# Optimization experiments

Measured on AMD Instinct MI355X. Metric: run time of the kernel, lower is better.

Reference implementation:

```python
import jax, jax.numpy as jnp
import numpy as np

D_HIST = 64
LO, HI = -3.0, 3.0
FALL_OFF = 0.02
EPS = 1e-6


def setup_inputs() -> dict:
    key = jax.random.key(0)
    k1, k2 = jax.random.split(key)
    x = jax.random.uniform(k1, (8, 3, 256, 256), dtype=jnp.float32)
    y = jax.random.uniform(k2, (8, 3, 256, 256), dtype=jnp.float32)
    return {"x": x, "y": y}


def _hist_feature(img):
    # img: (B, 3, H, W)
    B = img.shape[0]
    flat = (img + EPS).reshape(B, 3, -1)            # (B, 3, N)
    i_y = jnp.sqrt(jnp.sum(jnp.square(flat), axis=1))  # (B, N) pixel intensity
    lr, lg, lb = jnp.log(flat[:, 0]), jnp.log(flat[:, 1]), jnp.log(flat[:, 2])
    ur = lr - lg
    vr = lr - lb
    ug, vg = -ur, -ur + vr
    ub, vb = -vr, -vr + ur
    centers = jnp.linspace(LO, HI, D_HIST, dtype=img.dtype)  # (D,)

    def rbf(d):
        # inverse-quadratic kernel vs bin centers -> (B, N, D)
        return 1.0 / (1.0 + jnp.square(jnp.abs(d[..., None] - centers) / FALL_OFF))

    def hist_c(uc, vc):
        # weighted outer-product reduction over pixels (the bmm): (B, D, D)
        return jnp.einsum('bn,bnu,bnv->buv', i_y, rbf(uc), rbf(vc))

    hist = jnp.stack([hist_c(ur, vr), hist_c(ug, vg), hist_c(ub, vb)], axis=1)  # (B,3,D,D)
    total = jnp.sum(hist, axis=(1, 2, 3), keepdims=True)
    return hist / total


def reference(x, y):
    x_hist = _hist_feature(x)
    y_hist = _hist_feature(y)
    diff = jnp.sqrt(y_hist) - jnp.sqrt(x_hist)
    h = jnp.sum(jnp.square(diff), axis=(1, 2, 3))  # (B,)
    h_norm = jnp.sqrt(h) * jnp.sqrt(jnp.asarray(0.5, dtype=h.dtype))
    return jnp.mean(h_norm)
```

## Files before the change

kernel.cpp:

```cpp
#include <hip/hip_runtime.h>
#include <math.h>

#define N_PIX 65536
#define EPSF 1e-6f
#define CHUNKS 32
#define PX_PER_CHUNK 2048
#define PX_PER_WAVE 512
#define N_TILES (PX_PER_WAVE / 64)
#define N_JOBS 48
#define N_BLOCKS (N_JOBS * CHUNKS)
#define N_RBLOCKS (24 * 4)
#define LN2_50 34.65735903f

typedef __attribute__((ext_vector_type(2))) float f2;
using short8 = __attribute__((ext_vector_type(8))) short;
using f32x4  = __attribute__((ext_vector_type(4))) float;

__device__ __forceinline__ float rcp_fast(float x) { return __builtin_amdgcn_rcpf(x); }

#if __has_builtin(__builtin_amdgcn_cvt_pk_bf16_f32)
typedef __attribute__((ext_vector_type(2))) __bf16 bf16x2_t;
__device__ __forceinline__ uint32_t pk_bf16(float a, float b) {
    return __builtin_bit_cast(uint32_t, __builtin_amdgcn_cvt_pk_bf16_f32(a, b));
}
#else
__device__ __forceinline__ uint32_t pk_bf16(float a, float b) {
    const uint32_t ua = __builtin_bit_cast(uint32_t, a) + 0x8000u;
    const uint32_t ub = __builtin_bit_cast(uint32_t, b) + 0x8000u;
    return __builtin_amdgcn_perm(ub, ua, 0x07060302u);
}
#endif

__device__ __forceinline__ float4 phaseA(float pr, float pg, float pb, int c) {
    const float r  = pr + EPSF;
    const float g  = pg + EPSF;
    const float bl = pb + EPSF;
    const float wgt = sqrtf(fmaf(r, r, fmaf(g, g, bl * bl)));
    const float lr = __log2f(r), lg = __log2f(g), lb2 = __log2f(bl);
    const float l0 = (c == 0) ? lr : ((c == 1) ? lg : lb2);
    const float lu = (c == 0) ? lg : lr;
    const float lv = (c == 2) ? lg : lb2;
    return make_float4((l0 - lu) * LN2_50, (l0 - lv) * LN2_50, wgt, 0.0f);
}

__global__ __launch_bounds__(256, 4) void hist_kernel(
    const float* __restrict__ x, const float* __restrict__ y,
    float* __restrict__ partial, float* __restrict__ accum)
{
    const int blk = blockIdx.x;
    const int chunk = blk & (CHUNKS - 1);
    const int job = blk / CHUNKS;
    const int c = job % 3;
    const int ib = job / 3;
    const int img = ib >> 3;
    const int b = ib & 7;
    const float* __restrict__ src = (img == 0 ? x : y) + (size_t)b * 3 * N_PIX;

    const int tid = threadIdx.x;
    if (blk == 0 && tid < 25) ((unsigned*)accum)[tid] = 0u;

    __shared__ __align__(16) float lds[4096];
    const int lane = tid & 63;
    const int wv = tid >> 6;
    float* __restrict__ wbuf = lds + wv * 288;

    const int quad = lane >> 4;
    const int l15 = lane & 15;
    f2 ncb01, ncb23;
    {
        const float c0 = (-3.0f + (float)(l15)      * (6.0f / 63.0f)) * 50.0f;
        const float c1 = (-3.0f + (float)(16 + l15) * (6.0f / 63.0f)) * 50.0f;
        const float c2 = (-3.0f + (float)(32 + l15) * (6.0f / 63.0f)) * 50.0f;
        const float c3 = (-3.0f + (float)(48 + l15) * (6.0f / 63.0f)) * 50.0f;
        ncb01 = (f2){-c0, -c1};
        ncb23 = (f2){-c2, -c3};
    }
    const f2 one2 = {1.0f, 1.0f};

    f32x4 acc[16];
#pragma unroll
    for (int i = 0; i < 16; ++i) acc[i] = (f32x4){0.f, 0.f, 0.f, 0.f};

    const int px0 = chunk * PX_PER_CHUNK + wv * PX_PER_WAVE;

    float pr, pg, pb;
    {
        const int n = px0 + lane;
        pr = src[n]; pg = src[N_PIX + n]; pb = src[2 * N_PIX + n];
    }

#pragma unroll 1
    for (int st = 0; st < N_TILES; ++st) {
        const float4 uvw = phaseA(pr, pg, pb, c);
        *(float4*)(wbuf + lane * 4 + (lane >> 3) * 4) = uvw;

        if (st + 1 < N_TILES) {
            const int n2 = px0 + (st + 1) * 64 + lane;
            pr = src[n2]; pg = src[N_PIX + n2]; pb = src[2 * N_PIX + n2];
        }

#pragma unroll
        for (int h = 0; h < 2; ++h) {
            const int base = h * 32 + quad * 8;
            const float4* __restrict__ pbase =
                (const float4*)(wbuf + base * 4 + (base >> 3) * 4);
            int aU[4][4], aV[4][4];

#pragma unroll
            for (int jp = 0; jp < 4; ++jp) {
                const float4 pe = pbase[2 * jp];
                const float4 po = pbase[2 * jp + 1];

                f2 aue01, aue23, auo01, auo23;
                f2 bve01, bve23, bvo01, bvo23;
#pragma unroll
                for (int eo = 0; eo < 2; ++eo) {
                    const float ru = eo ? po.x : pe.x;
                    const float rv = eo ? po.y : pe.y;
                    const float rw = eo ? po.z : pe.z;
                    const f2 ru2 = {ru, ru}, rv2 = {rv, rv}, rw2 = {rw, rw};
                    const f2 tu01 = ru2 + ncb01, tu23 = ru2 + ncb23;
                    const f2 tv01 = rv2 + ncb01, tv23 = rv2 + ncb23;
                    const f2 qu01 = __builtin_elementwise_fma(tu01, tu01, one2);
                    const f2 qu23 = __builtin_elementwise_fma(tu23, tu23, one2);
                    const f2 qv01 = __builtin_elementwise_fma(tv01, tv01, one2);
                    const f2 qv23 = __builtin_elementwise_fma(tv23, tv23, one2);
                    const f2 au01 = (f2){rcp_fast(qu01.x), rcp_fast(qu01.y)} * rw2;
                    const f2 au23 = (f2){rcp_fast(qu23.x), rcp_fast(qu23.y)} * rw2;
                    const f2 bv01 = {rcp_fast(qv01.x), rcp_fast(qv01.y)};
                    const f2 bv23 = {rcp_fast(qv23.x), rcp_fast(qv23.y)};
                    if (eo) { auo01 = au01; auo23 = au23; bvo01 = bv01; bvo23 = bv23; }
                    else    { aue01 = au01; aue23 = au23; bve01 = bv01; bve23 = bv23; }
                }
                aU[0][jp] = pk_bf16(aue01.x, auo01.x);
                aU[1][jp] = pk_bf16(aue01.y, auo01.y);
                aU[2][jp] = pk_bf16(aue23.x, auo23.x);
                aU[3][jp] = pk_bf16(aue23.y, auo23.y);
                aV[0][jp] = pk_bf16(bve01.x, bvo01.x);
                aV[1][jp] = pk_bf16(bve01.y, bvo01.y);
                aV[2][jp] = pk_bf16(bve23.x, bvo23.x);
                aV[3][jp] = pk_bf16(bve23.y, bvo23.y);
            }

            short8 af[4], bf[4];
#pragma unroll
            for (int mt = 0; mt < 4; ++mt) {
                af[mt] = __builtin_bit_cast(short8,
                    make_int4(aU[mt][0], aU[mt][1], aU[mt][2], aU[mt][3]));
                bf[mt] = __builtin_bit_cast(short8,
                    make_int4(aV[mt][0], aV[mt][1], aV[mt][2], aV[mt][3]));
            }
#pragma unroll
            for (int mt = 0; mt < 4; ++mt)
#pragma unroll
                for (int nt = 0; nt < 4; ++nt)
                    acc[mt * 4 + nt] = __builtin_amdgcn_mfma_f32_16x16x32_bf16(
                        af[mt], bf[nt], acc[mt * 4 + nt], 0, 0, 0);
        }
    }

    float* __restrict__ outp = partial + (size_t)blk * 4096;
#pragma unroll 1
    for (int ch = 0; ch < 4; ++ch) {
        __syncthreads();
#pragma unroll
        for (int nt = 0; nt < 4; ++nt)
            *(f32x4*)(lds + wv * 1024 + nt * 256 + lane * 4) = acc[ch * 4 + nt];
        __syncthreads();
        const int e4 = tid * 4;
        const f32x4 s0 = *(const f32x4*)(lds +        e4);
        const f32x4 s1 = *(const f32x4*)(lds + 1024 + e4);
        const f32x4 s2 = *(const f32x4*)(lds + 2048 + e4);
        const f32x4 s3 = *(const f32x4*)(lds + 3072 + e4);
        const f32x4 s = (s0 + s1) + (s2 + s3);
        *(f32x4*)(outp + ch * 1024 + e4) = s;
    }
}

__global__ __launch_bounds__(256) void reduce_cross_kernel(
    const float* __restrict__ partial, float* __restrict__ accum,
    float* __restrict__ out)
{
    unsigned* __restrict__ ticket = (unsigned*)(accum + 24);
    const int jx = blockIdx.x >> 2;
    const int bb = jx / 3;
    const int e4 = (((blockIdx.x & 3) << 8) | threadIdx.x) * 4;
    const float* px = partial + (size_t)jx * CHUNKS * 4096 + e4;
    const float* py = partial + (size_t)(24 + jx) * CHUNKS * 4096 + e4;

    f32x4 qx = {0.f, 0.f, 0.f, 0.f}, qy = {0.f, 0.f, 0.f, 0.f};
#pragma unroll 8
    for (int k = 0; k < CHUNKS; ++k) {
        qx += *(const f32x4*)(px + (size_t)k * 4096);
        qy += *(const f32x4*)(py + (size_t)k * 4096);
    }
    float sx = (qx.x + qx.y) + (qx.z + qx.w);
    float sy = (qy.x + qy.y) + (qy.z + qy.w);
    float cr = (sqrtf(qx.x * qy.x) + sqrtf(qx.y * qy.y)) +
               (sqrtf(qx.z * qy.z) + sqrtf(qx.w * qy.w));

#pragma unroll
    for (int o = 32; o > 0; o >>= 1) {
        sx += __shfl_down(sx, o, 64);
        sy += __shfl_down(sy, o, 64);
        cr += __shfl_down(cr, o, 64);
    }
    __shared__ float red[12];
    const int wv = threadIdx.x >> 6;
    if ((threadIdx.x & 63) == 0) {
        red[wv] = sx; red[4 + wv] = sy; red[8 + wv] = cr;
    }
    __syncthreads();
    if (threadIdx.x == 0) {
        atomicAdd(&accum[bb],      red[0] + red[1] + red[2] + red[3]);
        atomicAdd(&accum[8 + bb],  red[4] + red[5] + red[6] + red[7]);
        atomicAdd(&accum[16 + bb], red[8] + red[9] + red[10] + red[11]);
        const unsigned old = __hip_atomic_fetch_add(ticket, 1u,
                                 __ATOMIC_ACQ_REL, __HIP_MEMORY_SCOPE_AGENT);
        if (old == N_RBLOCKS - 1) {
            float s = 0.0f;
#pragma unroll
            for (int b = 0; b < 8; ++b) {
                const float tx = __hip_atomic_load(&accum[b],      __ATOMIC_ACQUIRE, __HIP_MEMORY_SCOPE_AGENT);
                const float ty = __hip_atomic_load(&accum[8 + b],  __ATOMIC_ACQUIRE, __HIP_MEMORY_SCOPE_AGENT);
                const float cc = __hip_atomic_load(&accum[16 + b], __ATOMIC_ACQUIRE, __HIP_MEMORY_SCOPE_AGENT);
                const float rho = cc * __builtin_amdgcn_rsqf(tx * ty);
                s += sqrtf(fmaxf(1.0f - rho, 0.0f));
            }
            out[0] = s * 0.125f;
        }
    }
}

extern "C" void kernel_launch(void* const* d_in, const int* in_sizes, int n_in,
                              void* d_out, int out_size, void* d_ws, size_t ws_size,
                              hipStream_t stream)
{
    const float* x = (const float*)d_in[0];
    const float* y = (const float*)d_in[1];
    float* ws = (float*)d_ws;
    float* partial = ws;
    float* accum = ws + (size_t)N_BLOCKS * 4096;
    float* outf = (float*)d_out;

    hipLaunchKernelGGL(hist_kernel, dim3(N_BLOCKS), dim3(256), 0, stream,
                       x, y, partial, accum);
    hipLaunchKernelGGL(reduce_cross_kernel, dim3(N_RBLOCKS), dim3(256), 0, stream,
                       partial, accum, outf);
}
```

Measured before the change: 149.2 us.

## Split histogram output columns across waves and share U-side RBF tiles via LDS

Each wave now owns a 16-column slice of the 64x64 histogram, so it computes only one bin center's RBF values per pixel instead of four. The weighted U-side fragments are exchanged through double-buffered LDS across the four waves with block-level barriers. This removes the redundant 4x RBF/reciprocal work per wave, the cross-wave LDS reduction at the end, and most of the accumulator registers, which allows a higher occupancy target. In exchange it adds many __syncthreads and LDS traffic per macro-tile of 256 pixels.

```diff
diff --git a/kernel.cpp b/kernel.cpp
--- a/kernel.cpp
+++ b/kernel.cpp
@@ -5,8 +5,8 @@
 #define EPSF 1e-6f
 #define CHUNKS 32
 #define PX_PER_CHUNK 2048
-#define PX_PER_WAVE 512
-#define N_TILES (PX_PER_WAVE / 64)
+#define MACRO_PX 256
+#define N_MACROS 8
 #define N_JOBS 48
 #define N_BLOCKS (N_JOBS * CHUNKS)
 #define N_RBLOCKS (24 * 4)
@@ -43,7 +43,7 @@
     return make_float4((l0 - lu) * LN2_50, (l0 - lv) * LN2_50, wgt, 0.0f);
 }
 
-__global__ __launch_bounds__(256, 4) void hist_kernel(
+__global__ __launch_bounds__(256, 6) void hist_kernel(
     const float* __restrict__ x, const float* __restrict__ y,
     float* __restrict__ partial, float* __restrict__ accum)
 {
@@ -59,122 +59,112 @@
     const int tid = threadIdx.x;
     if (blk == 0 && tid < 25) ((unsigned*)accum)[tid] = 0u;
 
-    __shared__ __align__(16) float lds[4096];
+    __shared__ __align__(16) float uvw_lds[2][1152];
+    __shared__ __align__(16) int   af_lds[2][2048];
+
     const int lane = tid & 63;
     const int wv = tid >> 6;
-    float* __restrict__ wbuf = lds + wv * 288;
-
     const int quad = lane >> 4;
     const int l15 = lane & 15;
-    f2 ncb01, ncb23;
-    {
-        const float c0 = (-3.0f + (float)(l15)      * (6.0f / 63.0f)) * 50.0f;
-        const float c1 = (-3.0f + (float)(16 + l15) * (6.0f / 63.0f)) * 50.0f;
-        const float c2 = (-3.0f + (float)(32 + l15) * (6.0f / 63.0f)) * 50.0f;
-        const float c3 = (-3.0f + (float)(48 + l15) * (6.0f / 63.0f)) * 50.0f;
-        ncb01 = (f2){-c0, -c1};
-        ncb23 = (f2){-c2, -c3};
-    }
+
+    const float cc = (-3.0f + (float)(wv * 16 + l15) * (6.0f / 63.0f)) * 50.0f;
+    const f2 nc2 = {-cc, -cc};
     const f2 one2 = {1.0f, 1.0f};
 
-    f32x4 acc[16];
-#pragma unroll
-    for (int i = 0; i < 16; ++i) acc[i] = (f32x4){0.f, 0.f, 0.f, 0.f};
-
-    const int px0 = chunk * PX_PER_CHUNK + wv * PX_PER_WAVE;
+    f32x4 acc[4];
+#pragma unroll
+    for (int i = 0; i < 4; ++i) acc[i] = (f32x4){0.f, 0.f, 0.f, 0.f};
+
+    const int px0 = chunk * PX_PER_CHUNK;
 
     float pr, pg, pb;
     {
-        const int n = px0 + lane;
+        const int n = px0 + wv * 64 + lane;
         pr = src[n]; pg = src[N_PIX + n]; pb = src[2 * N_PIX + n];
     }
 
-#pragma unroll 1
-    for (int st = 0; st < N_TILES; ++st) {
-        const float4 uvw = phaseA(pr, pg, pb, c);
-        *(float4*)(wbuf + lane * 4 + (lane >> 3) * 4) = uvw;
-
-        if (st + 1 < N_TILES) {
-            const int n2 = px0 + (st + 1) * 64 + lane;
-            pr = src[n2]; pg = src[N_PIX + n2]; pb = src[2 * N_PIX + n2];
-        }
-
+    short8 bfh0, bfh1;
+
+    auto produce = [&](const float* __restrict__ ub, int s) {
+        const int bufsel = s & 1;
 #pragma unroll
         for (int h = 0; h < 2; ++h) {
-            const int base = h * 32 + quad * 8;
+            const int pxb = s * 64 + h * 32 + quad * 8;
             const float4* __restrict__ pbase =
-                (const float4*)(wbuf + base * 4 + (base >> 3) * 4);
-            int aU[4][4], aV[4][4];
-
+                (const float4*)(ub + pxb * 4 + (pxb >> 3) * 4);
+            int aw[4], bw[4];
 #pragma unroll
             for (int jp = 0; jp < 4; ++jp) {
                 const float4 pe = pbase[2 * jp];
                 const float4 po = pbase[2 * jp + 1];
-
-                f2 aue01, aue23, auo01, auo23;
-                f2 bve01, bve23, bvo01, bvo23;
-#pragma unroll
-                for (int eo = 0; eo < 2; ++eo) {
-                    const float ru = eo ? po.x : pe.x;
-                    const float rv = eo ? po.y : pe.y;
-                    const float rw = eo ? po.z : pe.z;
-                    const f2 ru2 = {ru, ru}, rv2 = {rv, rv}, rw2 = {rw, rw};
-                    const f2 tu01 = ru2 + ncb01, tu23 = ru2 + ncb23;
-                    const f2 tv01 = rv2 + ncb01, tv23 = rv2 + ncb23;
-                    const f2 qu01 = __builtin_elementwise_fma(tu01, tu01, one2);
-                    const f2 qu23 = __builtin_elementwise_fma(tu23, tu23, one2);
-                    const f2 qv01 = __builtin_elementwise_fma(tv01, tv01, one2);
-                    const f2 qv23 = __builtin_elementwise_fma(tv23, tv23, one2);
-                    const f2 au01 = (f2){rcp_fast(qu01.x), rcp_fast(qu01.y)} * rw2;
-                    const f2 au23 = (f2){rcp_fast(qu23.x), rcp_fast(qu23.y)} * rw2;
-                    const f2 bv01 = {rcp_fast(qv01.x), rcp_fast(qv01.y)};
-                    const f2 bv23 = {rcp_fast(qv23.x), rcp_fast(qv23.y)};
-                    if (eo) { auo01 = au01; auo23 = au23; bvo01 = bv01; bvo23 = bv23; }
-                    else    { aue01 = au01; aue23 = au23; bve01 = bv01; bve23 = bv23; }
-                }
-                aU[0][jp] = pk_bf16(aue01.x, auo01.x);
-                aU[1][jp] = pk_bf16(aue01.y, auo01.y);
-                aU[2][jp] = pk_bf16(aue23.x, auo23.x);
-                aU[3][jp] = pk_bf16(aue23.y, auo23.y);
-                aV[0][jp] = pk_bf16(bve01.x, bvo01.x);
-                aV[1][jp] = pk_bf16(bve01.y, bvo01.y);
-                aV[2][jp] = pk_bf16(bve23.x, bvo23.x);
-                aV[3][jp] = pk_bf16(bve23.y, bvo23.y);
+                const f2 ru2 = {pe.x, po.x};
+                const f2 rv2 = {pe.y, po.y};
+                const f2 rw2 = {pe.z, po.z};
+                const f2 tu = ru2 + nc2;
+                const f2 tv = rv2 + nc2;
+                const f2 qu = __builtin_elementwise_fma(tu, tu, one2);
+                const f2 qv = __builtin_elementwise_fma(tv, tv, one2);
+                const f2 au = (f2){rcp_fast(qu.x), rcp_fast(qu.y)} * rw2;
+                aw[jp] = (int)pk_bf16(au.x, au.y);
+                bw[jp] = (int)pk_bf16(rcp_fast(qv.x), rcp_fast(qv.y));
             }
-
-            short8 af[4], bf[4];
-#pragma unroll
-            for (int mt = 0; mt < 4; ++mt) {
+            *(int4*)(&af_lds[bufsel][h * 1024 + wv * 256 + lane * 4]) =
+                make_int4(aw[0], aw[1], aw[2], aw[3]);
+            const short8 bwv =
+                __builtin_bit_cast(short8, make_int4(bw[0], bw[1], bw[2], bw[3]));
+            if (h == 0) bfh0 = bwv; else bfh1 = bwv;
+        }
+    };
+    auto consume = [&](int s) {
+        const int bufsel = s & 1;
+#pragma unroll
+        for (int h = 0; h < 2; ++h) {
+            short8 af[4];
+#pragma unroll
+            for (int mt = 0; mt < 4; ++mt)
                 af[mt] = __builtin_bit_cast(short8,
-                    make_int4(aU[mt][0], aU[mt][1], aU[mt][2], aU[mt][3]));
-                bf[mt] = __builtin_bit_cast(short8,
-                    make_int4(aV[mt][0], aV[mt][1], aV[mt][2], aV[mt][3]));
-            }
+                    *(const int4*)(&af_lds[bufsel][h * 1024 + mt * 256 + lane * 4]));
+            const short8 bh = (h == 0) ? bfh0 : bfh1;
 #pragma unroll
             for (int mt = 0; mt < 4; ++mt)
-#pragma unroll
-                for (int nt = 0; nt < 4; ++nt)
-                    acc[mt * 4 + nt] = __builtin_amdgcn_mfma_f32_16x16x32_bf16(
-                        af[mt], bf[nt], acc[mt * 4 + nt], 0, 0, 0);
-        }
-    }
-
-    float* __restrict__ outp = partial + (size_t)blk * 4096;
+                acc[mt] = __builtin_amdgcn_mfma_f32_16x16x32_bf16(
+                    af[mt], bh, acc[mt], 0, 0, 0);
+        }
+    };
+
 #pragma unroll 1
-    for (int ch = 0; ch < 4; ++ch) {
-        __syncthreads();
-#pragma unroll
-        for (int nt = 0; nt < 4; ++nt)
-            *(f32x4*)(lds + wv * 1024 + nt * 256 + lane * 4) = acc[ch * 4 + nt];
-        __syncthreads();
-        const int e4 = tid * 4;
-        const f32x4 s0 = *(const f32x4*)(lds +        e4);
-        const f32x4 s1 = *(const f32x4*)(lds + 1024 + e4);
-        const f32x4 s2 = *(const f32x4*)(lds + 2048 + e4);
-        const f32x4 s3 = *(const f32x4*)(lds + 3072 + e4);
-        const f32x4 s = (s0 + s1) + (s2 + s3);
-        *(f32x4*)(outp + ch * 1024 + e4) = s;
-    }
+    for (int m = 0; m < N_MACROS; ++m) {
+        {
+            const float4 uvw = phaseA(pr, pg, pb, c);
+            const int pxw = wv * 64 + lane;
+            *(float4*)(&uvw_lds[m & 1][pxw * 4 + (pxw >> 3) * 4]) = uvw;
+        }
+        __syncthreads();
+
+        float nr = 0.f, ng = 0.f, nb = 0.f;
+        if (m + 1 < N_MACROS) {
+            const int n2 = px0 + (m + 1) * 256 + wv * 64 + lane;
+            nr = src[n2]; ng = src[N_PIX + n2]; nb = src[2 * N_PIX + n2];
+        }
+
+        const float* __restrict__ ub = &uvw_lds[m & 1][0];
+        produce(ub, 0);
+        __syncthreads();
+        consume(0); produce(ub, 1);
+        __syncthreads();
+        consume(1); produce(ub, 2);
+        __syncthreads();
+        consume(2); produce(ub, 3);
+        __syncthreads();
+        consume(3);
+
+        pr = nr; pg = ng; pb = nb;
+    }
+
+    float* __restrict__ outp = partial + (size_t)blk * 4096 + wv * 1024;
+#pragma unroll
+    for (int mt = 0; mt < 4; ++mt)
+        *(f32x4*)(outp + mt * 256 + lane * 4) = acc[mt];
 }
 
 __global__ __launch_bounds__(256) void reduce_cross_kernel(
```

New measurement: 154.7 us. 3.7% more time.

## Fuse cross-chunk reduction into histogram kernel via per-job last-block tickets

Applied to the files above, without the earlier changes.

Drops the separate reduction kernel. Each x/y job pair now gets a ticket counter, and the last of its 64 chunk blocks sums the partials and adds the Bhattacridge-style cross terms to the per-batch accumulators. A final ticket computes the output. The job index is remapped so x and y jobs for the same batch and channel sit next to each other. Accumulators are now zeroed with a memset before launch. This removes one kernel launch and its tail, but the reduction for each pair runs serially in a single block and adds a memset.

```diff
diff --git a/kernel.cpp b/kernel.cpp
--- a/kernel.cpp
+++ b/kernel.cpp
@@ -9,7 +9,6 @@
 #define N_TILES (PX_PER_WAVE / 64)
 #define N_JOBS 48
 #define N_BLOCKS (N_JOBS * CHUNKS)
-#define N_RBLOCKS (24 * 4)
 #define LN2_50 34.65735903f
 
 typedef __attribute__((ext_vector_type(2))) float f2;
@@ -45,21 +44,23 @@
 
 __global__ __launch_bounds__(256, 4) void hist_kernel(
     const float* __restrict__ x, const float* __restrict__ y,
-    float* __restrict__ partial, float* __restrict__ accum)
+    float* __restrict__ partial, float* __restrict__ accum,
+    float* __restrict__ out)
 {
     const int blk = blockIdx.x;
     const int chunk = blk & (CHUNKS - 1);
     const int job = blk / CHUNKS;
-    const int c = job % 3;
-    const int ib = job / 3;
-    const int img = ib >> 3;
-    const int b = ib & 7;
+    const int img = job & 1;
+    const int jp  = job >> 1;
+    const int c = jp % 3;
+    const int b = jp / 3;
     const float* __restrict__ src = (img == 0 ? x : y) + (size_t)b * 3 * N_PIX;
 
     const int tid = threadIdx.x;
-    if (blk == 0 && tid < 25) ((unsigned*)accum)[tid] = 0u;
 
     __shared__ __align__(16) float lds[4096];
+    __shared__ float red[12];
+    __shared__ unsigned last_flag;
     const int lane = tid & 63;
     const int wv = tid >> 6;
     float* __restrict__ wbuf = lds + wv * 288;
@@ -107,9 +108,9 @@
             int aU[4][4], aV[4][4];
 
 #pragma unroll
-            for (int jp = 0; jp < 4; ++jp) {
-                const float4 pe = pbase[2 * jp];
-                const float4 po = pbase[2 * jp + 1];
+            for (int jj = 0; jj < 4; ++jj) {
+                const float4 pe = pbase[2 * jj];
+                const float4 po = pbase[2 * jj + 1];
 
                 f2 aue01, aue23, auo01, auo23;
                 f2 bve01, bve23, bvo01, bvo23;
@@ -132,14 +133,14 @@
                     if (eo) { auo01 = au01; auo23 = au23; bvo01 = bv01; bvo23 = bv23; }
                     else    { aue01 = au01; aue23 = au23; bve01 = bv01; bve23 = bv23; }
                 }
-                aU[0][jp] = pk_bf16(aue01.x, auo01.x);
-                aU[1][jp] = pk_bf16(aue01.y, auo01.y);
-                aU[2][jp] = pk_bf16(aue23.x, auo23.x);
-                aU[3][jp] = pk_bf16(aue23.y, auo23.y);
-                aV[0][jp] = pk_bf16(bve01.x, bvo01.x);
-                aV[1][jp] = pk_bf16(bve01.y, bvo01.y);
-                aV[2][jp] = pk_bf16(bve23.x, bvo23.x);
-                aV[3][jp] = pk_bf16(bve23.y, bvo23.y);
+                aU[0][jj] = pk_bf16(aue01.x, auo01.x);
+                aU[1][jj] = pk_bf16(aue01.y, auo01.y);
+                aU[2][jj] = pk_bf16(aue23.x, auo23.x);
+                aU[3][jj] = pk_bf16(aue23.y, auo23.y);
+                aV[0][jj] = pk_bf16(bve01.x, bvo01.x);
+                aV[1][jj] = pk_bf16(bve01.y, bvo01.y);
+                aV[2][jj] = pk_bf16(bve23.x, bvo23.x);
+                aV[3][jj] = pk_bf16(bve23.y, bvo23.y);
             }
 
             short8 af[4], bf[4];
@@ -175,59 +176,64 @@
         const f32x4 s = (s0 + s1) + (s2 + s3);
         *(f32x4*)(outp + ch * 1024 + e4) = s;
     }
-}
-
-__global__ __launch_bounds__(256) void reduce_cross_kernel(
-    const float* __restrict__ partial, float* __restrict__ accum,
-    float* __restrict__ out)
-{
-    unsigned* __restrict__ ticket = (unsigned*)(accum + 24);
-    const int jx = blockIdx.x >> 2;
-    const int bb = jx / 3;
-    const int e4 = (((blockIdx.x & 3) << 8) | threadIdx.x) * 4;
-    const float* px = partial + (size_t)jx * CHUNKS * 4096 + e4;
-    const float* py = partial + (size_t)(24 + jx) * CHUNKS * 4096 + e4;
-
-    f32x4 qx = {0.f, 0.f, 0.f, 0.f}, qy = {0.f, 0.f, 0.f, 0.f};
-#pragma unroll 8
-    for (int k = 0; k < CHUNKS; ++k) {
-        qx += *(const f32x4*)(px + (size_t)k * 4096);
-        qy += *(const f32x4*)(py + (size_t)k * 4096);
-    }
-    float sx = (qx.x + qx.y) + (qx.z + qx.w);
-    float sy = (qy.x + qy.y) + (qy.z + qy.w);
-    float cr = (sqrtf(qx.x * qy.x) + sqrtf(qx.y * qy.y)) +
-               (sqrtf(qx.z * qy.z) + sqrtf(qx.w * qy.w));
-
-#pragma unroll
-    for (int o = 32; o > 0; o >>= 1) {
-        sx += __shfl_down(sx, o, 64);
-        sy += __shfl_down(sy, o, 64);
-        cr += __shfl_down(cr, o, 64);
-    }
-    __shared__ float red[12];
-    const int wv = threadIdx.x >> 6;
-    if ((threadIdx.x & 63) == 0) {
-        red[wv] = sx; red[4 + wv] = sy; red[8 + wv] = cr;
-    }
+
     __syncthreads();
-    if (threadIdx.x == 0) {
-        atomicAdd(&accum[bb],      red[0] + red[1] + red[2] + red[3]);
-        atomicAdd(&accum[8 + bb],  red[4] + red[5] + red[6] + red[7]);
-        atomicAdd(&accum[16 + bb], red[8] + red[9] + red[10] + red[11]);
-        const unsigned old = __hip_atomic_fetch_add(ticket, 1u,
+    unsigned* __restrict__ pticket = (unsigned*)(accum + 24);
+    if (tid == 0) {
+        const unsigned old = __hip_atomic_fetch_add(&pticket[jp], 1u,
                                  __ATOMIC_ACQ_REL, __HIP_MEMORY_SCOPE_AGENT);
-        if (old == N_RBLOCKS - 1) {
-            float s = 0.0f;
-#pragma unroll
-            for (int b = 0; b < 8; ++b) {
-                const float tx = __hip_atomic_load(&accum[b],      __ATOMIC_ACQUIRE, __HIP_MEMORY_SCOPE_AGENT);
-                const float ty = __hip_atomic_load(&accum[8 + b],  __ATOMIC_ACQUIRE, __HIP_MEMORY_SCOPE_AGENT);
-                const float cc = __hip_atomic_load(&accum[16 + b], __ATOMIC_ACQUIRE, __HIP_MEMORY_SCOPE_AGENT);
-                const float rho = cc * __builtin_amdgcn_rsqf(tx * ty);
-                s += sqrtf(fmaxf(1.0f - rho, 0.0f));
-            }
-            out[0] = s * 0.125f;
+        last_flag = (old == 63u) ? 1u : 0u;
+    }
+    __syncthreads();
+    if (last_flag) {
+        const float* __restrict__ px = partial + (size_t)(2 * jp) * CHUNKS * 4096;
+        const float* __restrict__ py = px + (size_t)CHUNKS * 4096;
+        float sx = 0.f, sy = 0.f, cr = 0.f;
+#pragma unroll 1
+        for (int s = 0; s < 4; ++s) {
+            const int e4 = tid * 4 + s * 1024;
+            const float* __restrict__ pxe = px + e4;
+            const float* __restrict__ pye = py + e4;
+            f32x4 qx = {0.f, 0.f, 0.f, 0.f}, qy = {0.f, 0.f, 0.f, 0.f};
+#pragma unroll 4
+            for (int k = 0; k < CHUNKS; ++k) {
+                qx += *(const f32x4*)(pxe + (size_t)k * 4096);
+                qy += *(const f32x4*)(pye + (size_t)k * 4096);
+            }
+            sx += (qx.x + qx.y) + (qx.z + qx.w);
+            sy += (qy.x + qy.y) + (qy.z + qy.w);
+            cr += (sqrtf(qx.x * qy.x) + sqrtf(qx.y * qy.y)) +
+                  (sqrtf(qx.z * qy.z) + sqrtf(qx.w * qy.w));
+        }
+#pragma unroll
+        for (int o = 32; o > 0; o >>= 1) {
+            sx += __shfl_down(sx, o, 64);
+            sy += __shfl_down(sy, o, 64);
+            cr += __shfl_down(cr, o, 64);
+        }
+        if ((tid & 63) == 0) {
+            red[wv] = sx; red[4 + wv] = sy; red[8 + wv] = cr;
+        }
+        __syncthreads();
+        if (tid == 0) {
+            atomicAdd(&accum[b],      red[0] + red[1] + red[2] + red[3]);
+            atomicAdd(&accum[8 + b],  red[4] + red[5] + red[6] + red[7]);
+            atomicAdd(&accum[16 + b], red[8] + red[9] + red[10] + red[11]);
+            unsigned* __restrict__ fin = (unsigned*)(accum + 48);
+            const unsigned old = __hip_atomic_fetch_add(fin, 1u,
+                                     __ATOMIC_ACQ_REL, __HIP_MEMORY_SCOPE_AGENT);
+            if (old == 23u) {
+                float sum = 0.0f;
+#pragma unroll
+                for (int bb = 0; bb < 8; ++bb) {
+                    const float tx = __hip_atomic_load(&accum[bb],      __ATOMIC_ACQUIRE, __HIP_MEMORY_SCOPE_AGENT);
+                    const float ty = __hip_atomic_load(&accum[8 + bb],  __ATOMIC_ACQUIRE, __HIP_MEMORY_SCOPE_AGENT);
+                    const float cc = __hip_atomic_load(&accum[16 + bb], __ATOMIC_ACQUIRE, __HIP_MEMORY_SCOPE_AGENT);
+                    const float rho = cc * __builtin_amdgcn_rsqf(tx * ty);
+                    sum += sqrtf(fmaxf(1.0f - rho, 0.0f));
+                }
+                out[0] = sum * 0.125f;
+            }
         }
     }
 }
@@ -243,8 +249,7 @@
     float* accum = ws + (size_t)N_BLOCKS * 4096;
     float* outf = (float*)d_out;
 
+    hipMemsetAsync(accum, 0, 49 * sizeof(float), stream);
     hipLaunchKernelGGL(hist_kernel, dim3(N_BLOCKS), dim3(256), 0, stream,
-                       x, y, partial, accum);
-    hipLaunchKernelGGL(reduce_cross_kernel, dim3(N_RBLOCKS), dim3(256), 0, stream,
-                       partial, accum, outf);
-}
+                       x, y, partial, accum, outf);
+}
```

Result: slower. 219.0 us (+46.8%).

## Accumulate per-chunk histograms atomically into a few slots per job

Applied to the files above, without the earlier changes.

Each hist block now atomically adds its 4096-bin partial histogram into one of 4 slots per job, where it used to write its own private partial buffer. The reduce kernel then reads only 4 slots per job instead of 32 chunks, which shrinks partial-buffer memory traffic. The cost is a memset of the slot buffer before the histogram kernel, plus global float atomics with contention from 8 blocks per slot. Float atomics also make the summation order nondeterministic.

```diff
diff --git a/kernel.cpp b/kernel.cpp
--- a/kernel.cpp
+++ b/kernel.cpp
@@ -9,6 +9,7 @@
 #define N_TILES (PX_PER_WAVE / 64)
 #define N_JOBS 48
 #define N_BLOCKS (N_JOBS * CHUNKS)
+#define SLOTS 4
 #define N_RBLOCKS (24 * 4)
 #define LN2_50 34.65735903f
 
@@ -45,7 +46,7 @@
 
 __global__ __launch_bounds__(256, 4) void hist_kernel(
     const float* __restrict__ x, const float* __restrict__ y,
-    float* __restrict__ partial, float* __restrict__ accum)
+    float* __restrict__ jobacc, float* __restrict__ accum)
 {
     const int blk = blockIdx.x;
     const int chunk = blk & (CHUNKS - 1);
@@ -57,7 +58,6 @@
     const float* __restrict__ src = (img == 0 ? x : y) + (size_t)b * 3 * N_PIX;
 
     const int tid = threadIdx.x;
-    if (blk == 0 && tid < 25) ((unsigned*)accum)[tid] = 0u;
 
     __shared__ __align__(16) float lds[4096];
     const int lane = tid & 63;
@@ -159,7 +159,8 @@
         }
     }
 
-    float* __restrict__ outp = partial + (size_t)blk * 4096;
+    float* __restrict__ outp =
+        jobacc + ((size_t)job * SLOTS + (chunk & (SLOTS - 1))) * 4096;
 #pragma unroll 1
     for (int ch = 0; ch < 4; ++ch) {
         __syncthreads();
@@ -173,26 +174,30 @@
         const f32x4 s2 = *(const f32x4*)(lds + 2048 + e4);
         const f32x4 s3 = *(const f32x4*)(lds + 3072 + e4);
         const f32x4 s = (s0 + s1) + (s2 + s3);
-        *(f32x4*)(outp + ch * 1024 + e4) = s;
+        float* __restrict__ dst = outp + ch * 1024 + e4;
+        atomicAdd(dst + 0, s.x);
+        atomicAdd(dst + 1, s.y);
+        atomicAdd(dst + 2, s.z);
+        atomicAdd(dst + 3, s.w);
     }
 }
 
 __global__ __launch_bounds__(256) void reduce_cross_kernel(
-    const float* __restrict__ partial, float* __restrict__ accum,
+    const float* __restrict__ jobacc, float* __restrict__ accum,
     float* __restrict__ out)
 {
     unsigned* __restrict__ ticket = (unsigned*)(accum + 24);
     const int jx = blockIdx.x >> 2;
     const int bb = jx / 3;
     const int e4 = (((blockIdx.x & 3) << 8) | threadIdx.x) * 4;
-    const float* px = partial + (size_t)jx * CHUNKS * 4096 + e4;
-    const float* py = partial + (size_t)(24 + jx) * CHUNKS * 4096 + e4;
+    const float* px = jobacc + (size_t)jx * SLOTS * 4096 + e4;
+    const float* py = jobacc + (size_t)(24 + jx) * SLOTS * 4096 + e4;
 
     f32x4 qx = {0.f, 0.f, 0.f, 0.f}, qy = {0.f, 0.f, 0.f, 0.f};
-#pragma unroll 8
-    for (int k = 0; k < CHUNKS; ++k) {
-        qx += *(const f32x4*)(px + (size_t)k * 4096);
-        qy += *(const f32x4*)(py + (size_t)k * 4096);
+#pragma unroll
+    for (int s = 0; s < SLOTS; ++s) {
+        qx += *(const f32x4*)(px + (size_t)s * 4096);
+        qy += *(const f32x4*)(py + (size_t)s * 4096);
     }
     float sx = (qx.x + qx.y) + (qx.z + qx.w);
     float sy = (qy.x + qy.y) + (qy.z + qy.w);
@@ -239,12 +244,14 @@
     const float* x = (const float*)d_in[0];
     const float* y = (const float*)d_in[1];
     float* ws = (float*)d_ws;
-    float* partial = ws;
-    float* accum = ws + (size_t)N_BLOCKS * 4096;
+    float* jobacc = ws;
+    float* accum = ws + (size_t)N_JOBS * SLOTS * 4096;
     float* outf = (float*)d_out;
 
+    hipMemsetAsync(ws, 0, ((size_t)N_JOBS * SLOTS * 4096 + 25) * sizeof(float),
+                   stream);
     hipLaunchKernelGGL(hist_kernel, dim3(N_BLOCKS), dim3(256), 0, stream,
-                       x, y, partial, accum);
+                       x, y, jobacc, accum);
     hipLaunchKernelGGL(reduce_cross_kernel, dim3(N_RBLOCKS), dim3(256), 0, stream,
-                       partial, accum, outf);
-}
+                       jobacc, accum, outf);
+}
```

After: 232.8 us. +56.0%, slower.
